# Optimization experiments

Hardware: AMD Instinct MI355X
Metric: run time of the kernel (lower is better)

The kernel has to match this reference:

```python
import jax, jax.numpy as jnp
import numpy as np

B = 8192          # batch (tokens)
D_IN = 4096       # in_features
D_OUT = 4096      # out_features
BS = 256          # block_size
K_IN = (D_IN + BS - 1) // BS
K_OUT = (D_OUT + BS - 1) // BS
INIT_SCALE = 0.1


def setup_inputs() -> dict:
    key = jax.random.key(0)
    k1, k2, k3, k4 = jax.random.split(key, 4)
    x = jax.random.normal(k1, (B, D_IN), dtype=jnp.float32)
    W = jax.random.normal(k2, (K_OUT, K_IN, BS), dtype=jnp.float32) * INIT_SCALE
    d_bernoulli = jnp.where(jax.random.bernoulli(k3, p=0.5, shape=(D_IN,)), 1.0, -1.0).astype(jnp.float32)
    bias = jax.random.normal(k4, (D_OUT,), dtype=jnp.float32) * INIT_SCALE
    return {"x": x, "W": W, "d_bernoulli": d_bernoulli, "bias": bias}


def _block_circulant_matmul(W, x, d):
    # W: (k_out, k_in, b); x: (batch, d_in); d: (d_in,) of +/-1
    batch = x.shape[0]
    k_out, k_in, b = W.shape
    x_d = x * d[None, :]
    pad_len = k_in * b - x.shape[-1]
    if pad_len > 0:
        x_d = jnp.pad(x_d, ((0, 0), (0, pad_len)))
    X_blocks = x_d.reshape(batch, k_in, b)          # (batch, k_in, b)
    X_fft = jnp.fft.fft(X_blocks, axis=-1)          # complex (batch, k_in, b)
    W_fft = jnp.fft.fft(W, axis=-1)                 # complex (k_out, k_in, b)
    # sum over k_in of X_fft * conj(W_fft[i]) for each output block i
    Y_fft = jnp.einsum('bjf,ijf->bif', X_fft, jnp.conjugate(W_fft))
    y = jnp.fft.ifft(Y_fft, axis=-1).real           # (batch, k_out, b)
    return y.reshape(batch, k_out * b)


def reference(x, W, d_bernoulli, bias):
    out = _block_circulant_matmul(W, x, d_bernoulli)
    out = out[..., :D_OUT]                          # truncate padded output blocks
    return out + bias[None, :]
```

## Files before the change

### kernel.cpp

```cpp
#include <hip/hip_runtime.h>


#define TWO_PI 6.283185307179586f
constexpr int RS = 304;

__device__ __forceinline__ int phys(int a) { return a + ((a >> 5) << 2); }

template<int SGN>
__device__ __forceinline__ void twmul(float& vr, float& vi, float c, float s)
{
    float r = vr * c + SGN * (vi * s);
    float i = vi * c - SGN * (vr * s);
    vr = r; vi = i;
}

template<int SGN>
__device__ __forceinline__ void pair1(float* __restrict__ Ar, float* __restrict__ Ai,
                                      int base, int u)
{
    float xr[16], xi[16];
#pragma unroll
    for (int s = 0; s < 16; ++s) {
        int a = base + phys(u + 16 * s);
        xr[s] = Ar[a];
        xi[s] = Ai[a];
    }
    float su, cu;
    __sincosf((float)u * (TWO_PI / 256.f), &su, &cu);
    const float CM[4] = {1.f, 0.92387953f, 0.70710678f, 0.38268343f};
    const float SM[4] = {0.f, 0.38268343f, 0.70710678f, 0.92387953f};
    float c1[4], s1[4], c2[4], s2[4], c3[4], s3[4];
#pragma unroll
    for (int m = 0; m < 4; ++m) {
        c1[m] = cu * CM[m] - su * SM[m];
        s1[m] = su * CM[m] + cu * SM[m];
        c2[m] = c1[m] * c1[m] - s1[m] * s1[m];
        s2[m] = 2.f * c1[m] * s1[m];
        c3[m] = c2[m] * c1[m] - s2[m] * s1[m];
        s3[m] = s2[m] * c1[m] + c2[m] * s1[m];
    }
#pragma unroll
    for (int m = 0; m < 4; ++m) {
        float t0r = xr[m] + xr[m + 8],       t0i = xi[m] + xi[m + 8];
        float t1r = xr[m] - xr[m + 8],       t1i = xi[m] - xi[m + 8];
        float t2r = xr[m + 4] + xr[m + 12],  t2i = xi[m + 4] + xi[m + 12];
        float t3r = xr[m + 4] - xr[m + 12],  t3i = xi[m + 4] - xi[m + 12];
        xr[m] = t0r + t2r;  xi[m] = t0i + t2i;
        float v1r = t1r + SGN * t3i, v1i = t1i - SGN * t3r;
        float v2r = t0r - t2r,       v2i = t0i - t2i;
        float v3r = t1r - SGN * t3i, v3i = t1i + SGN * t3r;
        twmul<SGN>(v1r, v1i, c1[m], s1[m]);
        twmul<SGN>(v2r, v2i, c2[m], s2[m]);
        twmul<SGN>(v3r, v3i, c3[m], s3[m]);
        xr[m + 4]  = v1r; xi[m + 4]  = v1i;
        xr[m + 8]  = v2r; xi[m + 8]  = v2i;
        xr[m + 12] = v3r; xi[m + 12] = v3i;
    }
    float cb1 = cu * cu - su * su, sb1 = 2.f * cu * su;
    { float c = cb1, s = sb1; cb1 = c * c - s * s; sb1 = 2.f * c * s; }
    float cb2 = cb1 * cb1 - sb1 * sb1, sb2 = 2.f * cb1 * sb1;
    float cb3 = cb2 * cb1 - sb2 * sb1, sb3 = sb2 * cb1 + cb2 * sb1;
#pragma unroll
    for (int k = 0; k < 4; ++k) {
        int s0 = 4 * k;
        float t0r = xr[s0] + xr[s0 + 2],     t0i = xi[s0] + xi[s0 + 2];
        float t1r = xr[s0] - xr[s0 + 2],     t1i = xi[s0] - xi[s0 + 2];
        float t2r = xr[s0 + 1] + xr[s0 + 3], t2i = xi[s0 + 1] + xi[s0 + 3];
        float t3r = xr[s0 + 1] - xr[s0 + 3], t3i = xi[s0 + 1] - xi[s0 + 3];
        xr[s0] = t0r + t2r;  xi[s0] = t0i + t2i;
        float v1r = t1r + SGN * t3i, v1i = t1i - SGN * t3r;
        float v2r = t0r - t2r,       v2i = t0i - t2i;
        float v3r = t1r - SGN * t3i, v3i = t1i + SGN * t3r;
        twmul<SGN>(v1r, v1i, cb1, sb1);
        twmul<SGN>(v2r, v2i, cb2, sb2);
        twmul<SGN>(v3r, v3i, cb3, sb3);
        xr[s0 + 1] = v1r; xi[s0 + 1] = v1i;
        xr[s0 + 2] = v2r; xi[s0 + 2] = v2i;
        xr[s0 + 3] = v3r; xi[s0 + 3] = v3i;
    }
#pragma unroll
    for (int s = 0; s < 16; ++s) {
        int a = base + phys(u + 16 * s);
        Ar[a] = xr[s]; Ai[a] = xi[s];
    }
}

template<int SGN, bool STORE_REV>
__device__ __forceinline__ void pair2(float* __restrict__ Ar, float* __restrict__ Ai,
                                      int base, int u)
{
    int a0 = base + 16 * u + ((u >> 1) << 2);
    float xr[16], xi[16];
#pragma unroll
    for (int v = 0; v < 4; ++v) {
        float4 vr = *(const float4*)(Ar + a0 + 4 * v);
        float4 vi = *(const float4*)(Ai + a0 + 4 * v);
        xr[4 * v] = vr.x; xr[4 * v + 1] = vr.y; xr[4 * v + 2] = vr.z; xr[4 * v + 3] = vr.w;
        xi[4 * v] = vi.x; xi[4 * v + 1] = vi.y; xi[4 * v + 2] = vi.z; xi[4 * v + 3] = vi.w;
    }
    const float CQ[4][4] = {
        {1.f, 1.f, 1.f, 1.f},
        {1.f, 0.92387953f, 0.70710678f, 0.38268343f},
        {1.f, 0.70710678f, 0.f, -0.70710678f},
        {1.f, 0.38268343f, -0.70710678f, -0.92387953f}};
    const float SQ[4][4] = {
        {0.f, 0.f, 0.f, 0.f},
        {0.f, 0.38268343f, 0.70710678f, 0.92387953f},
        {0.f, 0.70710678f, 1.f, 0.70710678f},
        {0.f, 0.92387953f, 0.70710678f, -0.38268343f}};
#pragma unroll
    for (int q = 0; q < 4; ++q) {
        float t0r = xr[q] + xr[q + 8],       t0i = xi[q] + xi[q + 8];
        float t1r = xr[q] - xr[q + 8],       t1i = xi[q] - xi[q + 8];
        float t2r = xr[q + 4] + xr[q + 12],  t2i = xi[q + 4] + xi[q + 12];
        float t3r = xr[q + 4] - xr[q + 12],  t3i = xi[q + 4] - xi[q + 12];
        xr[q] = t0r + t2r;  xi[q] = t0i + t2i;
        float v1r = t1r + SGN * t3i, v1i = t1i - SGN * t3r;
        float v2r = t0r - t2r,       v2i = t0i - t2i;
        float v3r = t1r - SGN * t3i, v3i = t1i + SGN * t3r;
        twmul<SGN>(v1r, v1i, CQ[q][1], SQ[q][1]);
        twmul<SGN>(v2r, v2i, CQ[q][2], SQ[q][2]);
        twmul<SGN>(v3r, v3i, CQ[q][3], SQ[q][3]);
        xr[q + 4]  = v1r; xi[q + 4]  = v1i;
        xr[q + 8]  = v2r; xi[q + 8]  = v2i;
        xr[q + 12] = v3r; xi[q + 12] = v3i;
    }
#pragma unroll
    for (int g = 0; g < 4; ++g) {
        int s0 = 4 * g;
        float t0r = xr[s0] + xr[s0 + 2],     t1r = xr[s0] - xr[s0 + 2];
        float t2r = xr[s0 + 1] + xr[s0 + 3], t3r = xr[s0 + 1] - xr[s0 + 3];
        float t0i = xi[s0] + xi[s0 + 2],     t1i = xi[s0] - xi[s0 + 2];
        float t2i = xi[s0 + 1] + xi[s0 + 3], t3i = xi[s0 + 1] - xi[s0 + 3];
        xr[s0]     = t0r + t2r;  xi[s0]     = t0i + t2i;
        xr[s0 + 1] = t1r + SGN * t3i;  xi[s0 + 1] = t1i - SGN * t3r;
        xr[s0 + 2] = t0r - t2r;        xi[s0 + 2] = t0i - t2i;
        xr[s0 + 3] = t1r - SGN * t3i;  xi[s0 + 3] = t1i + SGN * t3r;
    }
    if (STORE_REV) {
        int q2 = (u >> 2) + ((u & 3) << 2);
#pragma unroll
        for (int s = 0; s < 16; ++s) {
            int dest = q2 + ((s >> 2) << 4) + ((s & 3) << 6);
            int a = base + phys(dest);
            Ar[a] = xr[s]; Ai[a] = xi[s];
        }
    } else {
#pragma unroll
        for (int v = 0; v < 4; ++v) {
            *(float4*)(Ar + a0 + 4 * v) = make_float4(xr[4*v], xr[4*v+1], xr[4*v+2], xr[4*v+3]);
            *(float4*)(Ai + a0 + 4 * v) = make_float4(xi[4*v], xi[4*v+1], xi[4*v+2], xi[4*v+3]);
        }
    }
}

__global__ __launch_bounds__(256) void wfft_kernel(const float* __restrict__ W,
                                                   float* __restrict__ Wc4)
{
    __shared__ float wblk[256];
    __shared__ float tabc[256], tabs[256];
    int t   = threadIdx.x;
    int blk = blockIdx.x;
    wblk[t] = W[blk * 256 + t];
    float s, c;
    __sincosf((float)t * (TWO_PI / 256.f), &s, &c);
    tabc[t] = c; tabs[t] = s;
    __syncthreads();
    if (t <= 128) {
        float ar = 0.f, ai = 0.f;
        for (int cc = 0; cc < 256; ++cc) {
            int idx = (t * cc) & 255;
            float wv = wblk[cc];
            ar = fmaf(wv, tabc[idx], ar);
            ai = fmaf(wv, tabs[idx], ai);
        }
        int i = blk >> 4, j = blk & 15;
        int flat = ((i * 8 + (j >> 1)) * 132 + t) * 4 + ((j & 1) << 1);
        Wc4[flat]     = ar;
        Wc4[flat + 1] = ai;
    }
}

__global__ __launch_bounds__(256, 2)
void bc_kernel(const float* __restrict__ x,
               const float* __restrict__ d,
               const float* __restrict__ bias,
               const float* __restrict__ Wc4,
               float* __restrict__ out)
{
    __shared__ float Ar[16 * RS], Ai[16 * RS];
    int t  = threadIdx.x;
    int b0 = blockIdx.x * 2;
    int w = t >> 6, l = t & 63;
    int u = t & 15;
    int base = (t >> 4) * RS;

    const float4* d4 = (const float4*)d;
    const float4* x40 = (const float4*)(x + (size_t)b0 * 4096);
    const float4* x41 = (const float4*)(x + (size_t)(b0 + 1) * 4096);
#pragma unroll
    for (int it = 0; it < 4; ++it) {
        int idx = 256 * w + 64 * it + l;
        float4 dv = d4[idx];
        float4 v0 = x40[idx];
        float4 v1 = x41[idx];
        int a = (4 * w + it) * RS + 4 * l + ((l >> 3) << 2);
        *(float4*)(Ar + a) = make_float4(v0.x * dv.x, v0.y * dv.y, v0.z * dv.z, v0.w * dv.w);
        *(float4*)(Ai + a) = make_float4(v1.x * dv.x, v1.y * dv.y, v1.z * dv.z, v1.w * dv.w);
    }

    pair1<1>(Ar, Ai, base, u);
    pair2<1, true>(Ar, Ai, base, u);
    __syncthreads();

    {
        int f  = t & 127;
        int pf = phys(f);
        int pc = phys((256 - f) & 255);
        float zr[16], zi[16], z2r[16], z2i[16];
#pragma unroll
        for (int j = 0; j < 16; ++j) {
            zr[j]  = Ar[j * RS + pf];  zi[j]  = Ai[j * RS + pf];
            z2r[j] = Ar[j * RS + pc];  z2i[j] = Ai[j * RS + pc];
        }
        __syncthreads();

#pragma unroll
        for (int j = 0; j < 16; ++j) {
            float a = zr[j], b = zi[j], c = z2r[j], dd = z2i[j];
            zr[j]  = a + c;
            zi[j]  = b - dd;
            z2r[j] = b + dd;
            z2i[j] = c - a;
        }
        const float4* wb = (const float4*)Wc4;
        int ib = (t >> 7) * 8;
#pragma unroll
        for (int io = 0; io < 8; ++io) {
            int i = ib + io;
            float yr0 = 0.f, yi0 = 0.f, yr1 = 0.f, yi1 = 0.f;
#pragma unroll
            for (int jc = 0; jc < 8; ++jc) {
                float4 wv = wb[(i * 8 + jc) * 132 + f];
                int j0 = 2 * jc;
                yr0 = fmaf(zr[j0], wv.x, yr0);  yr0 = fmaf(-zi[j0], wv.y, yr0);
                yi0 = fmaf(zr[j0], wv.y, yi0);  yi0 = fmaf(zi[j0], wv.x, yi0);
                yr1 = fmaf(z2r[j0], wv.x, yr1); yr1 = fmaf(-z2i[j0], wv.y, yr1);
                yi1 = fmaf(z2r[j0], wv.y, yi1); yi1 = fmaf(z2i[j0], wv.x, yi1);
                yr0 = fmaf(zr[j0+1], wv.z, yr0);  yr0 = fmaf(-zi[j0+1], wv.w, yr0);
                yi0 = fmaf(zr[j0+1], wv.w, yi0);  yi0 = fmaf(zi[j0+1], wv.z, yi0);
                yr1 = fmaf(z2r[j0+1], wv.z, yr1); yr1 = fmaf(-z2i[j0+1], wv.w, yr1);
                yi1 = fmaf(z2r[j0+1], wv.w, yi1); yi1 = fmaf(z2i[j0+1], wv.z, yi1);
            }
            Ar[i * RS + pf] = yr0 - yi1;
            Ai[i * RS + pf] = yi0 + yr1;
            if (f >= 1) {
                Ar[i * RS + pc] = yr0 + yi1;
                Ai[i * RS + pc] = yr1 - yi0;
            }
        }
        if (t >= 64 && t < 80) {
            int i = t - 64;
            int p8 = phys(128);
            float yr0 = 0.f, yi0 = 0.f, yr1 = 0.f, yi1 = 0.f;
#pragma unroll
            for (int jc = 0; jc < 8; ++jc) {
                float4 wv = wb[(i * 8 + jc) * 132 + 128];
                int j0 = 2 * jc;
                float a0r = Ar[j0 * RS + p8],       a0i = Ai[j0 * RS + p8];
                float a1r = Ar[(j0 + 1) * RS + p8], a1i = Ai[(j0 + 1) * RS + p8];
                yr0 = fmaf(a0r, wv.x, yr0);   yi0 = fmaf(a0r, wv.y, yi0);
                yr1 = fmaf(a0i, wv.x, yr1);   yi1 = fmaf(a0i, wv.y, yi1);
                yr0 = fmaf(a1r, wv.z, yr0);   yi0 = fmaf(a1r, wv.w, yi0);
                yr1 = fmaf(a1i, wv.z, yr1);   yi1 = fmaf(a1i, wv.w, yi1);
            }
            Ar[i * RS + p8] = 2.f * (yr0 - yi1);
            Ai[i * RS + p8] = 2.f * (yi0 + yr1);
        }
    }
    __syncthreads();

    pair1<-1>(Ar, Ai, base, u);
    pair2<-1, false>(Ar, Ai, base, u);

    const float4* b4 = (const float4*)bias;
    float* o0 = out + (size_t)b0 * 4096;
    float* o1 = out + (size_t)(b0 + 1) * 4096;
    int dbase = ((l >> 4) & 3) + (((l >> 2) & 3) << 2) + ((l & 3) << 4);
#pragma unroll
    for (int it = 0; it < 4; ++it) {
        int idx = 256 * w + 64 * it + l;
        int rb  = (4 * w + it) * RS;
        float v0[4], v1[4];
#pragma unroll
        for (int e = 0; e < 4; ++e) {
            int a = rb + phys(dbase + (e << 6));
            v0[e] = Ar[a];
            v1[e] = Ai[a];
        }
        float4 bv = b4[idx];
        float4 ov0, ov1;
        ov0.x = v0[0] * (1.f / 512.f) + bv.x;
        ov0.y = v0[1] * (1.f / 512.f) + bv.y;
        ov0.z = v0[2] * (1.f / 512.f) + bv.z;
        ov0.w = v0[3] * (1.f / 512.f) + bv.w;
        ov1.x = v1[0] * (1.f / 512.f) + bv.x;
        ov1.y = v1[1] * (1.f / 512.f) + bv.y;
        ov1.z = v1[2] * (1.f / 512.f) + bv.z;
        ov1.w = v1[3] * (1.f / 512.f) + bv.w;
        ((float4*)o0)[idx] = ov0;
        ((float4*)o1)[idx] = ov1;
    }
}

extern "C" void kernel_launch(void* const* d_in, const int* in_sizes, int n_in,
                              void* d_out, int out_size, void* d_ws, size_t ws_size,
                              hipStream_t stream)
{
    const float* x    = (const float*)d_in[0];
    const float* W    = (const float*)d_in[1];
    const float* d    = (const float*)d_in[2];
    const float* bias = (const float*)d_in[3];
    float* out = (float*)d_out;
    float* Wc4 = (float*)d_ws;

    wfft_kernel<<<256, 256, 0, stream>>>(W, Wc4);
    bc_kernel<<<4096, 256, 0, stream>>>(x, d, bias, Wc4, out);
}
```

Baseline: 295.1 us.

## Replace padded shared-memory layout with XOR swizzle and drop intermediate barrier

Swaps the padded row stride (304 floats) for a dense 256-float row layout with an XOR swizzle. This shrinks LDS use per block and keeps bank conflicts low for the FFT passes, the spectral multiply and the output gather. The frequency-domain stage is remapped so that adjacent lanes of one wavefront share a frequency pair and split the output blocks between them. Because each frequency column is now read and written only within one wavefront, the __syncthreads between the spectral reads and writes is removed. This correctness depends on wavefront-lockstep execution, and the column-mapping change alters the access patterns to the global W spectrum.

```diff
diff --git a/kernel.cpp b/kernel.cpp
--- a/kernel.cpp
+++ b/kernel.cpp
@@ -2,9 +2,11 @@
 
 
 #define TWO_PI 6.283185307179586f
-constexpr int RS = 304;
-
-__device__ __forceinline__ int phys(int a) { return a + ((a >> 5) << 2); }
+
+__device__ __forceinline__ int swz(int r, int a)
+{
+    return (r << 8) + (a ^ ((a >> 3) & 28) ^ ((r & 1) << 4));
+}
 
 template<int SGN>
 __device__ __forceinline__ void twmul(float& vr, float& vi, float c, float s)
@@ -16,12 +18,12 @@
 
 template<int SGN>
 __device__ __forceinline__ void pair1(float* __restrict__ Ar, float* __restrict__ Ai,
-                                      int base, int u)
+                                      int reg, int u)
 {
     float xr[16], xi[16];
 #pragma unroll
     for (int s = 0; s < 16; ++s) {
-        int a = base + phys(u + 16 * s);
+        int a = swz(reg, u + 16 * s);
         xr[s] = Ar[a];
         xi[s] = Ai[a];
     }
@@ -80,21 +82,21 @@
     }
 #pragma unroll
     for (int s = 0; s < 16; ++s) {
-        int a = base + phys(u + 16 * s);
+        int a = swz(reg, u + 16 * s);
         Ar[a] = xr[s]; Ai[a] = xi[s];
     }
 }
 
 template<int SGN, bool STORE_REV>
 __device__ __forceinline__ void pair2(float* __restrict__ Ar, float* __restrict__ Ai,
-                                      int base, int u)
-{
-    int a0 = base + 16 * u + ((u >> 1) << 2);
+                                      int reg, int u)
+{
     float xr[16], xi[16];
 #pragma unroll
     for (int v = 0; v < 4; ++v) {
-        float4 vr = *(const float4*)(Ar + a0 + 4 * v);
-        float4 vi = *(const float4*)(Ai + a0 + 4 * v);
+        int a = swz(reg, 16 * u + 4 * v);
+        float4 vr = *(const float4*)(Ar + a);
+        float4 vi = *(const float4*)(Ai + a);
         xr[4 * v] = vr.x; xr[4 * v + 1] = vr.y; xr[4 * v + 2] = vr.z; xr[4 * v + 3] = vr.w;
         xi[4 * v] = vi.x; xi[4 * v + 1] = vi.y; xi[4 * v + 2] = vi.z; xi[4 * v + 3] = vi.w;
     }
@@ -142,14 +144,15 @@
 #pragma unroll
         for (int s = 0; s < 16; ++s) {
             int dest = q2 + ((s >> 2) << 4) + ((s & 3) << 6);
-            int a = base + phys(dest);
+            int a = swz(reg, dest);
             Ar[a] = xr[s]; Ai[a] = xi[s];
         }
     } else {
 #pragma unroll
         for (int v = 0; v < 4; ++v) {
-            *(float4*)(Ar + a0 + 4 * v) = make_float4(xr[4*v], xr[4*v+1], xr[4*v+2], xr[4*v+3]);
-            *(float4*)(Ai + a0 + 4 * v) = make_float4(xi[4*v], xi[4*v+1], xi[4*v+2], xi[4*v+3]);
+            int a = swz(reg, 16 * u + 4 * v);
+            *(float4*)(Ar + a) = make_float4(xr[4*v], xr[4*v+1], xr[4*v+2], xr[4*v+3]);
+            *(float4*)(Ai + a) = make_float4(xi[4*v], xi[4*v+1], xi[4*v+2], xi[4*v+3]);
         }
     }
 }
@@ -188,12 +191,12 @@
                const float* __restrict__ Wc4,
                float* __restrict__ out)
 {
-    __shared__ float Ar[16 * RS], Ai[16 * RS];
+    __shared__ float Ar[16 * 256], Ai[16 * 256];
     int t  = threadIdx.x;
     int b0 = blockIdx.x * 2;
     int w = t >> 6, l = t & 63;
     int u = t & 15;
-    int base = (t >> 4) * RS;
+    int reg = t >> 4;
 
     const float4* d4 = (const float4*)d;
     const float4* x40 = (const float4*)(x + (size_t)b0 * 4096);
@@ -204,27 +207,26 @@
         float4 dv = d4[idx];
         float4 v0 = x40[idx];
         float4 v1 = x41[idx];
-        int a = (4 * w + it) * RS + 4 * l + ((l >> 3) << 2);
+        int a = swz(4 * w + it, 4 * l);
         *(float4*)(Ar + a) = make_float4(v0.x * dv.x, v0.y * dv.y, v0.z * dv.z, v0.w * dv.w);
         *(float4*)(Ai + a) = make_float4(v1.x * dv.x, v1.y * dv.y, v1.z * dv.z, v1.w * dv.w);
     }
 
-    pair1<1>(Ar, Ai, base, u);
-    pair2<1, true>(Ar, Ai, base, u);
+    pair1<1>(Ar, Ai, reg, u);
+    pair2<1, true>(Ar, Ai, reg, u);
     __syncthreads();
 
     {
-        int f  = t & 127;
-        int pf = phys(f);
-        int pc = phys((256 - f) & 255);
+        int f  = (w << 5) + (l >> 1);
+        int ih = l & 1;
+        int cA = f;
+        int cB = (256 - f) & 255;
         float zr[16], zi[16], z2r[16], z2i[16];
 #pragma unroll
         for (int j = 0; j < 16; ++j) {
-            zr[j]  = Ar[j * RS + pf];  zi[j]  = Ai[j * RS + pf];
-            z2r[j] = Ar[j * RS + pc];  z2i[j] = Ai[j * RS + pc];
-        }
-        __syncthreads();
-
+            zr[j]  = Ar[swz(j, cA)];  zi[j]  = Ai[swz(j, cA)];
+            z2r[j] = Ar[swz(j, cB)];  z2i[j] = Ai[swz(j, cB)];
+        }
 #pragma unroll
         for (int j = 0; j < 16; ++j) {
             float a = zr[j], b = zi[j], c = z2r[j], dd = z2i[j];
@@ -234,7 +236,7 @@
             z2i[j] = c - a;
         }
         const float4* wb = (const float4*)Wc4;
-        int ib = (t >> 7) * 8;
+        int ib = ih * 8;
 #pragma unroll
         for (int io = 0; io < 8; ++io) {
             int i = ib + io;
@@ -252,36 +254,35 @@
                 yr1 = fmaf(z2r[j0+1], wv.z, yr1); yr1 = fmaf(-z2i[j0+1], wv.w, yr1);
                 yi1 = fmaf(z2r[j0+1], wv.w, yi1); yi1 = fmaf(z2i[j0+1], wv.z, yi1);
             }
-            Ar[i * RS + pf] = yr0 - yi1;
-            Ai[i * RS + pf] = yi0 + yr1;
+            Ar[swz(i, cA)] = yr0 - yi1;
+            Ai[swz(i, cA)] = yi0 + yr1;
             if (f >= 1) {
-                Ar[i * RS + pc] = yr0 + yi1;
-                Ai[i * RS + pc] = yr1 - yi0;
+                Ar[swz(i, cB)] = yr0 + yi1;
+                Ai[swz(i, cB)] = yr1 - yi0;
             }
         }
         if (t >= 64 && t < 80) {
             int i = t - 64;
-            int p8 = phys(128);
             float yr0 = 0.f, yi0 = 0.f, yr1 = 0.f, yi1 = 0.f;
 #pragma unroll
             for (int jc = 0; jc < 8; ++jc) {
                 float4 wv = wb[(i * 8 + jc) * 132 + 128];
                 int j0 = 2 * jc;
-                float a0r = Ar[j0 * RS + p8],       a0i = Ai[j0 * RS + p8];
-                float a1r = Ar[(j0 + 1) * RS + p8], a1i = Ai[(j0 + 1) * RS + p8];
+                float a0r = Ar[swz(j0, 128)],     a0i = Ai[swz(j0, 128)];
+                float a1r = Ar[swz(j0 + 1, 128)], a1i = Ai[swz(j0 + 1, 128)];
                 yr0 = fmaf(a0r, wv.x, yr0);   yi0 = fmaf(a0r, wv.y, yi0);
                 yr1 = fmaf(a0i, wv.x, yr1);   yi1 = fmaf(a0i, wv.y, yi1);
                 yr0 = fmaf(a1r, wv.z, yr0);   yi0 = fmaf(a1r, wv.w, yi0);
                 yr1 = fmaf(a1i, wv.z, yr1);   yi1 = fmaf(a1i, wv.w, yi1);
             }
-            Ar[i * RS + p8] = 2.f * (yr0 - yi1);
-            Ai[i * RS + p8] = 2.f * (yi0 + yr1);
+            Ar[swz(i, 128)] = 2.f * (yr0 - yi1);
+            Ai[swz(i, 128)] = 2.f * (yi0 + yr1);
         }
     }
     __syncthreads();
 
-    pair1<-1>(Ar, Ai, base, u);
-    pair2<-1, false>(Ar, Ai, base, u);
+    pair1<-1>(Ar, Ai, reg, u);
+    pair2<-1, false>(Ar, Ai, reg, u);
 
     const float4* b4 = (const float4*)bias;
     float* o0 = out + (size_t)b0 * 4096;
@@ -290,11 +291,11 @@
 #pragma unroll
     for (int it = 0; it < 4; ++it) {
         int idx = 256 * w + 64 * it + l;
-        int rb  = (4 * w + it) * RS;
+        int rg  = 4 * w + it;
         float v0[4], v1[4];
 #pragma unroll
         for (int e = 0; e < 4; ++e) {
-            int a = rb + phys(dbase + (e << 6));
+            int a = swz(rg, dbase + (e << 6));
             v0[e] = Ar[a];
             v1[e] = Ai[a];
         }
```

After: 294.0 us. No clear change (-0.4%).
